# Kernel optimization log

Hardware: AMD Instinct MI355X
Metric: run time of the kernel (lower is better)

## Reference

```python
import jax, jax.numpy as jnp
import numpy as np

B = 8192   # batch of independent theta draws (ABM calibration ensemble)
T = 4096   # recurrence length (__init__ T)
THETA_DIM = 11  # beta, g1..g4, b1..b4, sigma, r


def setup_inputs() -> dict:
    key = jax.random.key(0)
    k1, k2 = jax.random.split(key)
    # uniform[0,1) guarantees beta>0, sigma>0, r>=0 as asserted in the module
    theta = jax.random.uniform(k1, (B, THETA_DIM), dtype=jnp.float32)
    epsilons = jax.random.normal(k2, (B, T), dtype=jnp.float32)
    return {"theta": theta, "epsilons": epsilons}


def reference(theta, epsilons):
    # Brock-Hommes recurrence (Eqs. 39-40 of arXiv:2202.00625), vmapped over batch.
    beta = theta[:, 0]        # [B]
    g = theta[:, 1:5]         # [B,4]
    b = theta[:, 5:9]         # [B,4]
    sigma = theta[:, 9]       # [B]
    r = theta[:, 10]          # [B]
    R = 1.0 + r               # [B]

    def step(carry, eps_t):
        x1, x2, x3 = carry    # x[t-1], x[t-2], x[t-3], each [B]
        Rx2 = R * x2
        # exponent: [B,4]
        exponent = (beta * (x1 - Rx2))[:, None] * (g * x3[:, None] + b - Rx2[:, None])
        w = jax.nn.softmax(exponent, axis=-1)                 # [B,4]
        mean = jnp.sum(w * (g * x1[:, None] + b), axis=-1)    # [B]
        x_t = (mean + eps_t * sigma) / R                      # [B]
        return (x_t, x1, x2), x_t

    z = jnp.zeros(theta.shape[0], dtype=theta.dtype)
    # initial carry of zeros matches x[-1]=x[-2]=x[-3]=0 in the torch code
    _, xs = jax.lax.scan(step, (z, z, z), epsilons.T)  # xs: [T,B]
    return xs.T  # [B,T]
```

## Files before the change

### kernel.cpp

```cpp
#include <hip/hip_runtime.h>

#define THETA_DIM 11

typedef float v2f __attribute__((ext_vector_type(2)));

__device__ __forceinline__ v2f v2(float s) { return (v2f){s, s}; }

__global__ void __launch_bounds__(64, 1)
bh_kernel(const float* __restrict__ theta, const float* __restrict__ eps,
          float* __restrict__ out, int Tn) {
  const int b = blockIdx.x * 64 + threadIdx.x;

  const float* th = theta + (size_t)b * THETA_DIM;
  const float beta = th[0];
  const v2f g01 = {th[1], th[2]}, g23 = {th[3], th[4]};
  const v2f b01 = {th[5], th[6]}, b23 = {th[7], th[8]};
  const float sig = th[9];
  const float R   = 1.0f + th[10];
  const float invR = 1.0f / R;
  const float L2E  = 1.4426950408889634f;
  const float bl2e  = beta * L2E;
  const float bl2eR = bl2e * R;
  const float sR    = sig * invR;
  const v2f gR01 = g01 * v2(invR), gR23 = g23 * v2(invR);
  const v2f bR01 = b01 * v2(invR), bR23 = b23 * v2(invR);
  const v2f nR   = v2(-R);

  float x1 = 0.f, x2 = 0.f;
  float m1 = 0.f;
  v2f q01 = b01, q23 = b23;
  v2f c01 = bR01, c23 = bR23;
  v2f qmm;
  {
    v2f mx = __builtin_elementwise_max(q01, q23);
    v2f mn = __builtin_elementwise_min(q01, q23);
    qmm = (v2f){fmaxf(mx.x, mx.y), fminf(mn.x, mn.y)};
  }

  auto step = [&](float e) -> float {
    const float A  = fmaf(bl2e, x1, -m1);
    const v2f  uv  = v2(A) * qmm;
    const float m  = fmaxf(uv.x, uv.y);
    const v2f  e01 = __builtin_elementwise_fma(v2(A), q01, v2(-m));
    const v2f  e23 = __builtin_elementwise_fma(v2(A), q23, v2(-m));
    const v2f  p01 = {__builtin_amdgcn_exp2f(e01.x), __builtin_amdgcn_exp2f(e01.y)};
    const v2f  p23 = {__builtin_amdgcn_exp2f(e23.x), __builtin_amdgcn_exp2f(e23.y)};
    const v2f  w01  = __builtin_elementwise_fma(g01, v2(x2), b01);
    const v2f  w23  = __builtin_elementwise_fma(g23, v2(x2), b23);
    const v2f  q01n = __builtin_elementwise_fma(nR, v2(x1), w01);
    const v2f  q23n = __builtin_elementwise_fma(nR, v2(x1), w23);
    const v2f  mxv  = __builtin_elementwise_max(q01n, q23n);
    const v2f  mnv  = __builtin_elementwise_min(q01n, q23n);
    const float m1n = bl2eR * x1;
    const v2f  nv  = __builtin_elementwise_fma(p23, c23, p01 * c01);
    const float num = nv.x + nv.y;
    const v2f  dv  = p01 + p23;
    const float den = dv.x + dv.y;
    const float x  = fmaf(num, __builtin_amdgcn_rcpf(den), e * sR);
    x2 = x1; x1 = x;
    m1 = m1n; q01 = q01n; q23 = q23n;
    qmm = (v2f){fmaxf(mxv.x, mxv.y), fminf(mnv.x, mnv.y)};
    c01 = __builtin_elementwise_fma(gR01, v2(x), bR01);
    c23 = __builtin_elementwise_fma(gR23, v2(x), bR23);
    return x;
  };

  const float* ep = eps + (size_t)b * Tn;
  float* op = out + (size_t)b * Tn;

  float4 cA[4], cB[4], cC[4];
  #pragma unroll
  for (int i = 0; i < 4; ++i) cA[i] = *(const float4*)(ep + i * 4);
  #pragma unroll
  for (int i = 0; i < 4; ++i) cB[i] = *(const float4*)(ep + 16 + i * 4);

  const int NB = Tn / 16;
  int t0 = 0;
  for (int blk = 0; blk < NB; ++blk) {
    int tl = t0 + 32;
    if (tl > Tn - 16) tl = Tn - 16;
    const float* lp = ep + tl;
    #pragma unroll
    for (int i = 0; i < 4; ++i) cC[i] = *(const float4*)(lp + i * 4);

    #pragma unroll
    for (int i = 0; i < 4; ++i) {
      float4 o;
      o.x = step(cA[i].x);
      o.y = step(cA[i].y);
      o.z = step(cA[i].z);
      o.w = step(cA[i].w);
      *(float4*)(op + t0 + i * 4) = o;
    }

    #pragma unroll
    for (int i = 0; i < 4; ++i) { cA[i] = cB[i]; cB[i] = cC[i]; }
    t0 += 16;
  }
}

extern "C" void kernel_launch(void* const* d_in, const int* in_sizes, int n_in,
                              void* d_out, int out_size, void* d_ws, size_t ws_size,
                              hipStream_t stream) {
  const float* theta = (const float*)d_in[0];
  const float* eps   = (const float*)d_in[1];
  float* out = (float*)d_out;
  const int B  = in_sizes[0] / THETA_DIM;
  const int Tn = in_sizes[1] / B;
  const int blocks = B / 64;
  bh_kernel<<<blocks, 64, 0, stream>>>(theta, eps, out, Tn);
}
```

Measured before the change: 481.5 us.

## Split each chain's four softmax components across four lanes with DPP reductions

Each batch chain now runs on a group of four lanes, with one lane per softmax component. Sums and max/min across the four lanes use DPP quad permutes, and the launch grows from B/64 to B/16 blocks. This shortens each lane's serial work per step and puts four times as many wavefronts on the GPU. In exchange, every step gains extra cross-lane DPP operations on the critical path, all four lanes load the same eps values, and only one lane in four writes output.

New measurement: 475.5 us. Within noise of the previous version (-1.2%).

```diff
diff --git a/kernel.cpp b/kernel.cpp
--- a/kernel.cpp
+++ b/kernel.cpp
@@ -2,19 +2,26 @@
 
 #define THETA_DIM 11
 
-typedef float v2f __attribute__((ext_vector_type(2)));
-
-__device__ __forceinline__ v2f v2(float s) { return (v2f){s, s}; }
+__device__ __forceinline__ float dpp_xor1(float v) {
+  return __builtin_bit_cast(float,
+    __builtin_amdgcn_update_dpp(0, __builtin_bit_cast(int, v), 0xB1, 0xF, 0xF, true));
+}
+__device__ __forceinline__ float dpp_xor2(float v) {
+  return __builtin_bit_cast(float,
+    __builtin_amdgcn_update_dpp(0, __builtin_bit_cast(int, v), 0x4E, 0xF, 0xF, true));
+}
 
 __global__ void __launch_bounds__(64, 1)
 bh_kernel(const float* __restrict__ theta, const float* __restrict__ eps,
           float* __restrict__ out, int Tn) {
-  const int b = blockIdx.x * 64 + threadIdx.x;
+  const int tid = threadIdx.x;
+  const int chain = blockIdx.x * 16 + (tid >> 2);
+  const int j = tid & 3;
 
-  const float* th = theta + (size_t)b * THETA_DIM;
+  const float* th = theta + (size_t)chain * THETA_DIM;
   const float beta = th[0];
-  const v2f g01 = {th[1], th[2]}, g23 = {th[3], th[4]};
-  const v2f b01 = {th[5], th[6]}, b23 = {th[7], th[8]};
+  const float g  = th[1 + j];
+  const float bb = th[5 + j];
   const float sig = th[9];
   const float R   = 1.0f + th[10];
   const float invR = 1.0f / R;
@@ -22,51 +29,48 @@
   const float bl2e  = beta * L2E;
   const float bl2eR = bl2e * R;
   const float sR    = sig * invR;
-  const v2f gR01 = g01 * v2(invR), gR23 = g23 * v2(invR);
-  const v2f bR01 = b01 * v2(invR), bR23 = b23 * v2(invR);
-  const v2f nR   = v2(-R);
+  const float gR = g * invR, bR = bb * invR;
+  const float nR = -R;
 
   float x1 = 0.f, x2 = 0.f;
   float m1 = 0.f;
-  v2f q01 = b01, q23 = b23;
-  v2f c01 = bR01, c23 = bR23;
-  v2f qmm;
+  float q  = bb;
+  float c  = bR;
+  float qmax, qmin;
   {
-    v2f mx = __builtin_elementwise_max(q01, q23);
-    v2f mn = __builtin_elementwise_min(q01, q23);
-    qmm = (v2f){fmaxf(mx.x, mx.y), fminf(mn.x, mn.y)};
+    float t  = dpp_xor1(q);
+    float mx = fmaxf(q, t), mn = fminf(q, t);
+    qmax = fmaxf(mx, dpp_xor2(mx));
+    qmin = fminf(mn, dpp_xor2(mn));
   }
 
   auto step = [&](float e) -> float {
     const float A  = fmaf(bl2e, x1, -m1);
-    const v2f  uv  = v2(A) * qmm;
-    const float m  = fmaxf(uv.x, uv.y);
-    const v2f  e01 = __builtin_elementwise_fma(v2(A), q01, v2(-m));
-    const v2f  e23 = __builtin_elementwise_fma(v2(A), q23, v2(-m));
-    const v2f  p01 = {__builtin_amdgcn_exp2f(e01.x), __builtin_amdgcn_exp2f(e01.y)};
-    const v2f  p23 = {__builtin_amdgcn_exp2f(e23.x), __builtin_amdgcn_exp2f(e23.y)};
-    const v2f  w01  = __builtin_elementwise_fma(g01, v2(x2), b01);
-    const v2f  w23  = __builtin_elementwise_fma(g23, v2(x2), b23);
-    const v2f  q01n = __builtin_elementwise_fma(nR, v2(x1), w01);
-    const v2f  q23n = __builtin_elementwise_fma(nR, v2(x1), w23);
-    const v2f  mxv  = __builtin_elementwise_max(q01n, q23n);
-    const v2f  mnv  = __builtin_elementwise_min(q01n, q23n);
+    const float m  = fmaxf(A * qmax, A * qmin);
+    const float eo = fmaf(A, q, -m);
+    const float p  = __builtin_amdgcn_exp2f(eo);
+    const float pc = p * c;
+    float den = p  + dpp_xor1(p);
+    float num = pc + dpp_xor1(pc);
+    den += dpp_xor2(den);
+    num += dpp_xor2(num);
+    const float w  = fmaf(g, x2, bb);
+    const float qn = fmaf(nR, x1, w);
+    float t  = dpp_xor1(qn);
+    float mx = fmaxf(qn, t), mn = fminf(qn, t);
+    mx = fmaxf(mx, dpp_xor2(mx));
+    mn = fminf(mn, dpp_xor2(mn));
     const float m1n = bl2eR * x1;
-    const v2f  nv  = __builtin_elementwise_fma(p23, c23, p01 * c01);
-    const float num = nv.x + nv.y;
-    const v2f  dv  = p01 + p23;
-    const float den = dv.x + dv.y;
-    const float x  = fmaf(num, __builtin_amdgcn_rcpf(den), e * sR);
+    const float x = fmaf(num, __builtin_amdgcn_rcpf(den), e * sR);
     x2 = x1; x1 = x;
-    m1 = m1n; q01 = q01n; q23 = q23n;
-    qmm = (v2f){fmaxf(mxv.x, mxv.y), fminf(mnv.x, mnv.y)};
-    c01 = __builtin_elementwise_fma(gR01, v2(x), bR01);
-    c23 = __builtin_elementwise_fma(gR23, v2(x), bR23);
+    q = qn; qmax = mx; qmin = mn; m1 = m1n;
+    c = fmaf(gR, x, bR);
     return x;
   };
 
-  const float* ep = eps + (size_t)b * Tn;
-  float* op = out + (size_t)b * Tn;
+  const float* ep = eps + (size_t)chain * Tn;
+  float* op = out + (size_t)chain * Tn;
+  const bool writer = (j == 0);
 
   float4 cA[4], cB[4], cC[4];
   #pragma unroll
@@ -90,7 +94,7 @@
       o.y = step(cA[i].y);
       o.z = step(cA[i].z);
       o.w = step(cA[i].w);
-      *(float4*)(op + t0 + i * 4) = o;
+      if (writer) *(float4*)(op + t0 + i * 4) = o;
     }
 
     #pragma unroll
@@ -107,6 +111,6 @@
   float* out = (float*)d_out;
   const int B  = in_sizes[0] / THETA_DIM;
   const int Tn = in_sizes[1] / B;
-  const int blocks = B / 64;
+  const int blocks = B / 16;
   bh_kernel<<<blocks, 64, 0, stream>>>(theta, eps, out, Tn);
 }
```
